# Optimization experiments

Hardware: AMD Instinct MI355X
Metric: run time of the kernel (lower is better)

Reference implementation:

```python
import jax, jax.numpy as jnp
import numpy as np

LEAKY_SLOPE = 0.01  # torch F.leaky_relu default


def _l2norm(x):
    # matches F.normalize(p=2, dim=-1, eps=1e-12)
    n = jnp.linalg.norm(x, axis=-1, keepdims=True)
    return x / jnp.maximum(n, 1e-12)


def setup_inputs() -> dict:
    key = jax.random.key(0)
    k1, k2, k3, k4 = jax.random.split(key, 4)
    B, S, H = 16, 256, 768
    return {
        "query_embs": jax.random.normal(k1, (B, S, H), dtype=jnp.float32),
        "key_embs": jax.random.normal(k2, (2 * B, S, H), dtype=jnp.float32),
        "logit_scale": jnp.log(jnp.asarray(1.0 / 0.07, dtype=jnp.float32)),
        "alpha_raw": jnp.asarray(1.0, dtype=jnp.float32),
        "q_mask": jax.random.randint(k3, (B, S), 0, 2).astype(jnp.int32),
        "k_mask": jax.random.randint(k4, (2 * B, S), 0, 2).astype(jnp.int32),
    }


def reference(query_embs, key_embs, logit_scale, alpha_raw, q_mask, k_mask):
    q = _l2norm(query_embs)                 # [B, S, H]
    k = _l2norm(key_embs)                   # [2B, S, H]
    S = q.shape[1]

    # all-pairs token similarity: [B, 2B, S, S]
    sim = jnp.einsum('ish,jth->ijst', q, k)

    # exponential distance weighting
    pos = jnp.arange(S)
    dist = jnp.abs(pos[:, None] - pos[None, :]).astype(sim.dtype)
    alpha = jax.nn.leaky_relu(alpha_raw, LEAKY_SLOPE)
    sim = sim * jnp.exp(-alpha * dist)

    # joint validity mask: q_mask[i,s] & k_mask[j,t]
    valid = (q_mask[:, None, :, None] * k_mask[None, :, None, :]) > 0

    logits = jnp.where(valid, jnp.exp(logit_scale) * sim, -jnp.inf)
    p = jnp.nan_to_num(jax.nn.softmax(logits, axis=-1), nan=0.0)  # fully-masked rows -> 0

    # softmax-weighted aggregation of key tokens, then dot with query tokens
    agg = jnp.einsum('ijst,jth->ijsh', p, k)        # [B, 2B, S, H]
    per_tok = jnp.einsum('ish,ijsh->ijs', q, agg)   # [B, 2B, S]
    per_tok = per_tok * q_mask[:, None, :].astype(per_tok.dtype)
    return per_tok.sum(axis=-1)                     # [B, 2B]
```

## Files before the change

kernel.cpp:

```cpp
#include <hip/hip_runtime.h>
#include <hip/hip_bf16.h>

#define BQ   16
#define BK2  32
#define SEQ  256
#define HD   768

typedef __attribute__((ext_vector_type(8))) short bf16x8;
typedef __attribute__((ext_vector_type(4))) float f32x4;

__device__ __forceinline__ void glds16(const unsigned short* g, unsigned short* l) {
    __builtin_amdgcn_global_load_lds(
        (const __attribute__((address_space(1))) unsigned int*)g,
        (__attribute__((address_space(3))) unsigned int*)l, 16, 0, 0);
}

__device__ __forceinline__ unsigned int pack2_bf16(float a, float b) {
    unsigned ua = __float_as_uint(a), ub = __float_as_uint(b);
    ua += 0x7FFFu + ((ua >> 16) & 1u);
    ub += 0x7FFFu + ((ub >> 16) & 1u);
    return (ua >> 16) | (ub & 0xFFFF0000u);
}

__global__ __launch_bounds__(256) void norm_kernel(
    const float* __restrict__ q, const float* __restrict__ k,
    unsigned short* __restrict__ qn, unsigned short* __restrict__ kn,
    float* __restrict__ out)
{
    if (blockIdx.x == 0 && threadIdx.x < 256) {
        out[threadIdx.x] = 0.f; out[threadIdx.x + 256] = 0.f;
    }
    int row  = blockIdx.x * 4 + (threadIdx.x >> 6);
    int lane = threadIdx.x & 63;
    const int NQ = BQ * SEQ;
    const float* src = (row < NQ) ? q + (size_t)row * HD
                                  : k + (size_t)(row - NQ) * HD;
    unsigned int* dst = (unsigned int*)((row < NQ) ? qn + (size_t)row * HD
                                                   : kn + (size_t)(row - NQ) * HD);
    float4 v[3];
    float ss = 0.f;
#pragma unroll
    for (int c = 0; c < 3; ++c) {
        v[c] = ((const float4*)src)[lane + 64 * c];
        ss += v[c].x * v[c].x + v[c].y * v[c].y + v[c].z * v[c].z + v[c].w * v[c].w;
    }
#pragma unroll
    for (int m = 1; m < 64; m <<= 1) ss += __shfl_xor(ss, m, 64);
    float inv = rsqrtf(fmaxf(ss, 1e-24f));
#pragma unroll
    for (int c = 0; c < 3; ++c) {
        uint2 o = make_uint2(pack2_bf16(v[c].x * inv, v[c].y * inv),
                             pack2_bf16(v[c].z * inv, v[c].w * inv));
        ((uint2*)dst)[lane + 64 * c] = o;
    }
}

__global__ __launch_bounds__(512, 2) void li_kernel(
    const unsigned short* __restrict__ qn, const unsigned short* __restrict__ kn,
    const float* __restrict__ g_ls, const float* __restrict__ g_ar,
    const int* __restrict__ q_mask, const int* __restrict__ k_mask,
    float* __restrict__ out)
{
    const int j  = blockIdx.x, i = blockIdx.y, sh = blockIdx.z;
    const int tid  = threadIdx.x;
    const int w    = tid >> 6, lane = tid & 63;
    const int ln   = lane & 15, lg = lane >> 4;
    const int wsd  = w >> 2, wt = w & 3;

    __shared__ __align__(16) unsigned short As[128 * 64];
    __shared__ __align__(16) unsigned short Bs[256 * 64];
    __shared__ float w2[SEQ];
    __shared__ float kmB[SEQ];
    __shared__ float red[8];

    float a0 = g_ar[0];
    float alpha = (a0 > 0.f) ? a0 : 0.01f * a0;
    float scale = __expf(g_ls[0]);
    if (tid < 256) w2[tid] = scale * __expf(-alpha * (float)tid);
    else           kmB[tid - 256] = (k_mask[j * SEQ + (tid - 256)] != 0) ? 1.f : 0.f;

    const int rl  = lane >> 3;
    const int gch = (lane & 7) ^ rl;
    const unsigned short* aq = qn + ((size_t)i * SEQ + sh * 128 + w * 8 + rl) * HD + gch * 8;
    const unsigned short* bq = kn + ((size_t)j * SEQ + w * 8 + rl) * HD + gch * 8;
    unsigned short* al = As + (w * 8) * 64;
    unsigned short* bl = Bs + (w * 8) * 64;

    f32x4 acc[4][4];
    const f32x4 zero4 = {0.f, 0.f, 0.f, 0.f};
#pragma unroll
    for (int a = 0; a < 4; ++a)
#pragma unroll
        for (int b = 0; b < 4; ++b) acc[a][b] = zero4;

    for (int kk = 0; kk < HD; kk += 64) {
        __syncthreads();
        glds16(aq + kk,           al);
        glds16(aq + kk + 64 * HD, al + 64 * 64);
#pragma unroll
        for (int c = 0; c < 4; ++c)
            glds16(bq + kk + c * (64 * HD), bl + c * (64 * 64));
        __syncthreads();
        const bf16x8* A8 = (const bf16x8*)As;
        const bf16x8* B8 = (const bf16x8*)Bs;
#pragma unroll
        for (int ks = 0; ks < 2; ++ks) {
            const int ch = (ks * 4 + lg) ^ (ln & 7);
            bf16x8 af[4], bfr[4];
#pragma unroll
            for (int rm = 0; rm < 4; ++rm)
                af[rm] = A8[(wsd * 64 + rm * 16 + ln) * 8 + ch];
#pragma unroll
            for (int cn = 0; cn < 4; ++cn)
                bfr[cn] = B8[(wt * 64 + cn * 16 + ln) * 8 + ch];
#pragma unroll
            for (int rm = 0; rm < 4; ++rm)
#pragma unroll
                for (int cn = 0; cn < 4; ++cn)
                    acc[rm][cn] = __builtin_amdgcn_mfma_f32_16x16x32_bf16(
                        af[rm], bfr[cn], acc[rm][cn], 0, 0, 0);
        }
    }

    __syncthreads();
    float* zs  = (float*)As;
    float* wsc = zs + 512;

#pragma unroll
    for (int rm = 0; rm < 4; ++rm)
#pragma unroll
        for (int r = 0; r < 4; ++r) {
            int srow = wsd * 64 + rm * 16 + lg * 4 + r;
            int s  = sh * 128 + srow;
            float ze = 0.f, we = 0.f;
#pragma unroll
            for (int cn = 0; cn < 4; ++cn) {
                int t = wt * 64 + cn * 16 + ln;
                float sim = acc[rm][cn][r];
                int d = s - t; d = (d < 0) ? -d : d;
                float e = kmB[t] * __expf(sim * w2[d]);
                ze += e;
                we = fmaf(e, sim, we);
            }
#pragma unroll
            for (int m = 1; m < 16; m <<= 1) {
                ze += __shfl_xor(ze, m, 64);
                we += __shfl_xor(we, m, 64);
            }
            if (ln == 0) { zs[srow * 4 + wt] = ze; wsc[srow * 4 + wt] = we; }
        }
    __syncthreads();

    float part = 0.f;
    if (tid < 128) {
        const float4 Z4 = ((const float4*)zs)[tid];
        const float4 W4 = ((const float4*)wsc)[tid];
        float Z = Z4.x + Z4.y + Z4.z + Z4.w;
        float W = W4.x + W4.y + W4.z + W4.w;
        float pt = (Z > 0.f) ? (W / Z) : 0.f;
        part = pt * (float)q_mask[i * SEQ + sh * 128 + tid];
    }
#pragma unroll
    for (int m = 1; m < 64; m <<= 1) part += __shfl_xor(part, m, 64);
    if (lane == 0) red[w] = part;
    __syncthreads();
    if (tid == 0) {
        float tot = red[0] + red[1] + red[2] + red[3]
                  + red[4] + red[5] + red[6] + red[7];
        atomicAdd(&out[i * BK2 + j], tot);
    }
}

extern "C" void kernel_launch(void* const* d_in, const int* in_sizes, int n_in,
                              void* d_out, int out_size, void* d_ws, size_t ws_size,
                              hipStream_t stream) {
    const float* q  = (const float*)d_in[0];
    const float* k  = (const float*)d_in[1];
    const float* ls = (const float*)d_in[2];
    const float* ar = (const float*)d_in[3];
    const int* qm   = (const int*)d_in[4];
    const int* km   = (const int*)d_in[5];
    float* out      = (float*)d_out;

    unsigned short* qn = (unsigned short*)d_ws;
    unsigned short* kn = qn + (size_t)BQ * SEQ * HD;

    norm_kernel<<<(BQ + BK2) * SEQ / 4, 256, 0, stream>>>(q, k, qn, kn, (float*)d_out);
    li_kernel<<<dim3(BK2, BQ, 2), 512, 0, stream>>>(qn, kn, ls, ar, qm, km, (float*)d_out);
}
```

Before: 145.6 us.

## Double-buffer LDS tiles with async global-to-LDS prefetch two stages ahead

Makes the shared-memory A/B tiles double-buffered and issues the global_load_lds copies for k-tile kt+2 while tile kt is being consumed, waiting on vmcnt instead of a full syncthreads before each compute step. All LDS fragments are loaded before the MFMA block, and the MFMAs run with raised wave priority. This targets the global-load latency that was fully exposed in the single-buffered loop. In exchange LDS use doubles to about 48KB+ per block, which may limit occupancy at two blocks per CU, and correctness relies on hand-written waitcnt counts.

```diff
diff --git a/kernel.cpp b/kernel.cpp
--- a/kernel.cpp
+++ b/kernel.cpp
@@ -5,6 +5,7 @@
 #define BK2  32
 #define SEQ  256
 #define HD   768
+#define NKT  12
 
 typedef __attribute__((ext_vector_type(8))) short bf16x8;
 typedef __attribute__((ext_vector_type(4))) float f32x4;
@@ -67,8 +68,8 @@
     const int ln   = lane & 15, lg = lane >> 4;
     const int wsd  = w >> 2, wt = w & 3;
 
-    __shared__ __align__(16) unsigned short As[128 * 64];
-    __shared__ __align__(16) unsigned short Bs[256 * 64];
+    __shared__ __align__(16) unsigned short As[2 * 128 * 64];
+    __shared__ __align__(16) unsigned short Bs[2 * 256 * 64];
     __shared__ float w2[SEQ];
     __shared__ float kmB[SEQ];
     __shared__ float red[8];
@@ -83,8 +84,20 @@
     const int gch = (lane & 7) ^ rl;
     const unsigned short* aq = qn + ((size_t)i * SEQ + sh * 128 + w * 8 + rl) * HD + gch * 8;
     const unsigned short* bq = kn + ((size_t)j * SEQ + w * 8 + rl) * HD + gch * 8;
-    unsigned short* al = As + (w * 8) * 64;
-    unsigned short* bl = Bs + (w * 8) * 64;
+    unsigned short* alw = As + (w * 8) * 64;
+    unsigned short* blw = Bs + (w * 8) * 64;
+
+#define STAGE(kt, b) do {                                            \
+        const int kk_ = (kt) * 64;                                   \
+        unsigned short* al_ = alw + (b) * (128 * 64);                \
+        unsigned short* bl_ = blw + (b) * (256 * 64);                \
+        glds16(aq + kk_,            al_);                            \
+        glds16(aq + kk_ + 64 * HD,  al_ + 64 * 64);                  \
+        glds16(bq + kk_,            bl_);                            \
+        glds16(bq + kk_ + 64 * HD,  bl_ + 64 * 64);                  \
+        glds16(bq + kk_ + 128 * HD, bl_ + 128 * 64);                 \
+        glds16(bq + kk_ + 192 * HD, bl_ + 192 * 64);                 \
+    } while (0)
 
     f32x4 acc[4][4];
     const f32x4 zero4 = {0.f, 0.f, 0.f, 0.f};
@@ -93,34 +106,45 @@
 #pragma unroll
         for (int b = 0; b < 4; ++b) acc[a][b] = zero4;
 
-    for (int kk = 0; kk < HD; kk += 64) {
-        __syncthreads();
-        glds16(aq + kk,           al);
-        glds16(aq + kk + 64 * HD, al + 64 * 64);
-#pragma unroll
-        for (int c = 0; c < 4; ++c)
-            glds16(bq + kk + c * (64 * HD), bl + c * (64 * 64));
-        __syncthreads();
-        const bf16x8* A8 = (const bf16x8*)As;
-        const bf16x8* B8 = (const bf16x8*)Bs;
+    STAGE(0, 0);
+    STAGE(1, 1);
+
+    for (int kt = 0; kt < NKT; ++kt) {
+        const int cur = kt & 1;
+        if (kt == NKT - 1) asm volatile("s_waitcnt vmcnt(0)" ::: "memory");
+        else               asm volatile("s_waitcnt vmcnt(6)" ::: "memory");
+        __builtin_amdgcn_sched_barrier(0);
+        __builtin_amdgcn_s_barrier();
+
+        const bf16x8* A8 = (const bf16x8*)(As + cur * (128 * 64));
+        const bf16x8* B8 = (const bf16x8*)(Bs + cur * (256 * 64));
+        bf16x8 af[2][4], bfr[2][4];
 #pragma unroll
         for (int ks = 0; ks < 2; ++ks) {
             const int ch = (ks * 4 + lg) ^ (ln & 7);
-            bf16x8 af[4], bfr[4];
 #pragma unroll
             for (int rm = 0; rm < 4; ++rm)
-                af[rm] = A8[(wsd * 64 + rm * 16 + ln) * 8 + ch];
+                af[ks][rm] = A8[(wsd * 64 + rm * 16 + ln) * 8 + ch];
 #pragma unroll
             for (int cn = 0; cn < 4; ++cn)
-                bfr[cn] = B8[(wt * 64 + cn * 16 + ln) * 8 + ch];
+                bfr[ks][cn] = B8[(wt * 64 + cn * 16 + ln) * 8 + ch];
+        }
+
+        __builtin_amdgcn_s_setprio(1);
+#pragma unroll
+        for (int ks = 0; ks < 2; ++ks)
 #pragma unroll
             for (int rm = 0; rm < 4; ++rm)
 #pragma unroll
                 for (int cn = 0; cn < 4; ++cn)
                     acc[rm][cn] = __builtin_amdgcn_mfma_f32_16x16x32_bf16(
-                        af[rm], bfr[cn], acc[rm][cn], 0, 0, 0);
-        }
-    }
+                        af[ks][rm], bfr[ks][cn], acc[rm][cn], 0, 0, 0);
+        __builtin_amdgcn_s_setprio(0);
+
+        __builtin_amdgcn_s_barrier();
+        if (kt + 2 < NKT) STAGE(kt + 2, cur);
+    }
+#undef STAGE
 
     __syncthreads();
     float* zs  = (float*)As;
```

Result: slower. 160.0 us (+9.9%).

## Double-buffer LDS K-tiles with async prefetch and XCD-aware block mapping

Applied to the files above, without the earlier changes.

Replaces the single-buffered 64-wide K loop with a two-stage LDS ring of 32-wide K tiles. The next tile is loaded by global_load_lds while MFMAs run on the current one, using explicit vmcnt waits and raw barriers. The grid is flattened and remapped so that blocks sharing the same key batch land on the same XCD, which should improve L2 reuse. It also raises wave priority around the MFMA burst. In exchange the code depends on hand-tuned waitcnt ordering, and the swizzle changes along with the tile shape.

```diff
diff --git a/kernel.cpp b/kernel.cpp
--- a/kernel.cpp
+++ b/kernel.cpp
@@ -5,6 +5,7 @@
 #define BK2  32
 #define SEQ  256
 #define HD   768
+#define NKT  24
 
 typedef __attribute__((ext_vector_type(8))) short bf16x8;
 typedef __attribute__((ext_vector_type(4))) float f32x4;
@@ -61,14 +62,19 @@
     const int* __restrict__ q_mask, const int* __restrict__ k_mask,
     float* __restrict__ out)
 {
-    const int j  = blockIdx.x, i = blockIdx.y, sh = blockIdx.z;
+    const int bid = blockIdx.x;
+    const int xcd = bid & 7, local = bid >> 3;
+    const int j  = xcd * 4 + (local >> 5);
+    const int i  = (local >> 1) & 15;
+    const int sh = local & 1;
+
     const int tid  = threadIdx.x;
     const int w    = tid >> 6, lane = tid & 63;
     const int ln   = lane & 15, lg = lane >> 4;
     const int wsd  = w >> 2, wt = w & 3;
 
-    __shared__ __align__(16) unsigned short As[128 * 64];
-    __shared__ __align__(16) unsigned short Bs[256 * 64];
+    __shared__ __align__(16) unsigned short As[2 * 128 * 32];
+    __shared__ __align__(16) unsigned short Bs[2 * 256 * 32];
     __shared__ float w2[SEQ];
     __shared__ float kmB[SEQ];
     __shared__ float red[8];
@@ -79,12 +85,17 @@
     if (tid < 256) w2[tid] = scale * __expf(-alpha * (float)tid);
     else           kmB[tid - 256] = (k_mask[j * SEQ + (tid - 256)] != 0) ? 1.f : 0.f;
 
-    const int rl  = lane >> 3;
-    const int gch = (lane & 7) ^ rl;
-    const unsigned short* aq = qn + ((size_t)i * SEQ + sh * 128 + w * 8 + rl) * HD + gch * 8;
-    const unsigned short* bq = kn + ((size_t)j * SEQ + w * 8 + rl) * HD + gch * 8;
-    unsigned short* al = As + (w * 8) * 64;
-    unsigned short* bl = Bs + (w * 8) * 64;
+    const int srow = lane >> 2;
+    const int gch  = (lane & 3) ^ ((srow >> 1) & 3);
+    const unsigned short* aq = qn + ((size_t)i * SEQ + sh * 128 + w * 16 + srow) * HD + gch * 8;
+    const unsigned short* bq = kn + ((size_t)j * SEQ + w * 32 + srow) * HD + gch * 8;
+
+#define STAGE(kt, b) do {                                            \
+        const int kk_ = (kt) * 32;                                   \
+        glds16(aq + kk_,           As + (b) * 4096 + w * 512);       \
+        glds16(bq + kk_,           Bs + (b) * 8192 + w * 1024);      \
+        glds16(bq + kk_ + 16 * HD, Bs + (b) * 8192 + w * 1024 + 512);\
+    } while (0)
 
     f32x4 acc[4][4];
     const f32x4 zero4 = {0.f, 0.f, 0.f, 0.f};
@@ -93,34 +104,47 @@
 #pragma unroll
         for (int b = 0; b < 4; ++b) acc[a][b] = zero4;
 
-    for (int kk = 0; kk < HD; kk += 64) {
-        __syncthreads();
-        glds16(aq + kk,           al);
-        glds16(aq + kk + 64 * HD, al + 64 * 64);
-#pragma unroll
-        for (int c = 0; c < 4; ++c)
-            glds16(bq + kk + c * (64 * HD), bl + c * (64 * 64));
-        __syncthreads();
-        const bf16x8* A8 = (const bf16x8*)As;
-        const bf16x8* B8 = (const bf16x8*)Bs;
-#pragma unroll
-        for (int ks = 0; ks < 2; ++ks) {
-            const int ch = (ks * 4 + lg) ^ (ln & 7);
-            bf16x8 af[4], bfr[4];
-#pragma unroll
-            for (int rm = 0; rm < 4; ++rm)
-                af[rm] = A8[(wsd * 64 + rm * 16 + ln) * 8 + ch];
-#pragma unroll
-            for (int cn = 0; cn < 4; ++cn)
-                bfr[cn] = B8[(wt * 64 + cn * 16 + ln) * 8 + ch];
-#pragma unroll
-            for (int rm = 0; rm < 4; ++rm)
-#pragma unroll
-                for (int cn = 0; cn < 4; ++cn)
-                    acc[rm][cn] = __builtin_amdgcn_mfma_f32_16x16x32_bf16(
-                        af[rm], bfr[cn], acc[rm][cn], 0, 0, 0);
-        }
-    }
+    STAGE(0, 0);
+    STAGE(1, 1);
+
+    const int rsw = (ln >> 1) & 3;
+
+#define COMPUTE(A8, B8) do {                                               \
+        bf16x8 af[4], bfr[4];                                              \
+        _Pragma("unroll")                                                  \
+        for (int cn = 0; cn < 4; ++cn)                                     \
+            bfr[cn] = (B8)[(wt * 64 + cn * 16 + ln) * 4 + (lg ^ rsw)];     \
+        _Pragma("unroll")                                                  \
+        for (int rm = 0; rm < 4; ++rm)                                     \
+            af[rm] = (A8)[(wsd * 64 + rm * 16 + ln) * 4 + (lg ^ rsw)];     \
+        __builtin_amdgcn_s_setprio(1);                                     \
+        _Pragma("unroll")                                                  \
+        for (int rm = 0; rm < 4; ++rm)                                     \
+            _Pragma("unroll")                                              \
+            for (int cn = 0; cn < 4; ++cn)                                 \
+                acc[rm][cn] = __builtin_amdgcn_mfma_f32_16x16x32_bf16(     \
+                    af[rm], bfr[cn], acc[rm][cn], 0, 0, 0);                \
+        __builtin_amdgcn_s_setprio(0);                                     \
+    } while (0)
+
+#pragma unroll 1
+    for (int kt = 0; kt < NKT; kt += 2) {
+        asm volatile("s_waitcnt vmcnt(3)" ::: "memory");
+        __builtin_amdgcn_sched_barrier(0);
+        __builtin_amdgcn_s_barrier();
+        COMPUTE((const bf16x8*)As, (const bf16x8*)Bs);
+        __builtin_amdgcn_s_barrier();
+        if (kt + 2 < NKT) STAGE(kt + 2, 0);
+        if (kt + 2 < NKT) asm volatile("s_waitcnt vmcnt(3)" ::: "memory");
+        else              asm volatile("s_waitcnt vmcnt(0)" ::: "memory");
+        __builtin_amdgcn_sched_barrier(0);
+        __builtin_amdgcn_s_barrier();
+        COMPUTE((const bf16x8*)(As + 4096), (const bf16x8*)(Bs + 8192));
+        __builtin_amdgcn_s_barrier();
+        if (kt + 3 < NKT) STAGE(kt + 3, 1);
+    }
+#undef COMPUTE
+#undef STAGE
 
     __syncthreads();
     float* zs  = (float*)As;
@@ -186,5 +210,5 @@
     unsigned short* kn = qn + (size_t)BQ * SEQ * HD;
 
     norm_kernel<<<(BQ + BK2) * SEQ / 4, 256, 0, stream>>>(q, k, qn, kn, (float*)d_out);
-    li_kernel<<<dim3(BK2, BQ, 2), 512, 0, stream>>>(qn, kn, ls, ar, qm, km, (float*)d_out);
-}
+    li_kernel<<<BK2 * BQ * 2, 512, 0, stream>>>(qn, kn, ls, ar, qm, km, (float*)d_out);
+}
```

New measurement: 151.1 us. +3.8%, slower.
